# Kernel tuning notes

Measured on AMD Instinct MI355X. Metric: run time of the kernel, lower is better.

Reference implementation:

```python
import jax, jax.numpy as jnp
import numpy as np

BITS = (2, 4, 8)
GROUP = 4
EPS = 1e-5


def _ste_round(x):
    return x + jax.lax.stop_gradient(jnp.round(x) - x)


def _quant_act(x, b):
    s = float(2 ** b - 1)
    return _ste_round(jnp.clip(x, 0.0, 1.0) * s) / s


def _quant_weight(w, mean, std, b):
    # normalize by (mean, std) of the gating-selected channels, then b-bit uniform quant on [-1, 1]
    wn = jnp.clip((w - mean) / (std + EPS), -1.0, 1.0)
    s = float(2 ** b - 1)
    u = _ste_round((wn + 1.0) * 0.5 * s) / s
    return 2.0 * u - 1.0


def _mixed_qconv(x, w, w_mean, w_std, w_logits, a_logits):
    # bitwidth-selectable conv: softmax mixture over quantized weights / activations
    pw = jax.nn.softmax(w_logits)
    pa = jax.nn.softmax(a_logits)
    w_mix = sum(pw[i] * _quant_weight(w, w_mean, w_std, b) for i, b in enumerate(BITS))
    x_mix = sum(pa[i] * _quant_act(x, b) for i, b in enumerate(BITS))
    return jax.lax.conv_general_dilated(
        x_mix, w_mix, window_strides=(1, 1), padding='SAME',
        dimension_numbers=('NCHW', 'OIHW', 'NCHW'))


def _bn(x, g, b, m, v):
    inv = jax.lax.rsqrt(v + EPS)
    return (x - m[None, :, None, None]) * (g * inv)[None, :, None, None] + b[None, :, None, None]


def _masked_mean_std(w, mask):
    # mean/std over gate-selected filter slices; torch uses .data -> stop_gradient, unbiased std
    m = jnp.broadcast_to(mask, w.shape)
    cnt = jnp.sum(m)
    mean = jnp.sum(w * m) / cnt
    var = jnp.sum(m * (w - mean) ** 2) / (cnt - 1.0)
    return jax.lax.stop_gradient(mean), jax.lax.stop_gradient(jnp.sqrt(var))


def _indicator(w1, thr):
    n, c, h, wk = w1.shape
    fw = w1.reshape(n // GROUP, GROUP * c * h * wk)
    nf = fw / jnp.max(jnp.abs(fw))
    norm = jnp.sum(jnp.abs(nf), axis=1) / (GROUP * c * h * wk)  # [n_choices]
    soft = jax.nn.sigmoid(norm - thr)
    hard = (norm > thr).astype(w1.dtype)
    return hard - jax.lax.stop_gradient(soft) + soft  # STE indicator


def setup_inputs() -> dict:
    key = jax.random.key(0)
    ks = jax.random.split(key, 10)
    B, C, H, W = 64, 256, 32, 32
    return {
        'x': jax.random.normal(ks[0], (B, C, H, W), jnp.float32),
        'w1': jax.random.normal(ks[1], (C, C, 3, 3), jnp.float32) * 0.05,
        'w2': jax.random.normal(ks[2], (C, C, 3, 3), jnp.float32) * 0.05,
        'bn1_gamma': jnp.ones((C,), jnp.float32),
        'bn1_beta': jnp.zeros((C,), jnp.float32),
        'bn1_mean': jax.random.normal(ks[3], (C,), jnp.float32) * 0.1,
        'bn1_var': jax.random.uniform(ks[4], (C,), jnp.float32, 0.5, 1.5),
        'bn2_gamma': jnp.ones((C,), jnp.float32),
        'bn2_beta': jnp.zeros((C,), jnp.float32),
        'bn2_mean': jax.random.normal(ks[5], (C,), jnp.float32) * 0.1,
        'bn2_var': jax.random.uniform(ks[6], (C,), jnp.float32, 0.5, 1.5),
        'threshold': jnp.zeros((1,), jnp.float32),
        'w_logits1': jax.random.normal(ks[7], (3,), jnp.float32) * 0.1,
        'a_logits1': jax.random.normal(ks[8], (3,), jnp.float32) * 0.1,
        'w_logits2': jax.random.normal(ks[9], (3,), jnp.float32) * 0.1,
        'a_logits2': jnp.zeros((3,), jnp.float32),
    }


def reference(x, w1, w2, bn1_gamma, bn1_beta, bn1_mean, bn1_var,
              bn2_gamma, bn2_beta, bn2_mean, bn2_var, threshold,
              w_logits1, a_logits1, w_logits2, a_logits2):
    thr = threshold[0]
    ind = _indicator(w1, thr)                       # [n_choices]
    ind_ch = jnp.repeat(ind, GROUP)                 # [out_plane]
    gate_mask = jax.lax.stop_gradient((ind_ch > 0).astype(x.dtype))

    # both_preact path
    residual = x
    h = jax.nn.relu(_bn(x, bn1_gamma, bn1_beta, bn1_mean, bn1_var))
    m1, s1 = _masked_mean_std(w1, gate_mask[:, None, None, None])
    h = _mixed_qconv(h, w1, m1, s1, w_logits1, a_logits1)
    h = jax.nn.relu(_bn(h, bn2_gamma, bn2_beta, bn2_mean, bn2_var))
    m2, s2 = _masked_mean_std(w2, gate_mask[None, :, None, None])
    h = h * ind_ch[None, :, None, None]             # differentiable channel gating
    h = _mixed_qconv(h, w2, m2, s2, w_logits2, a_logits2)
    return h + residual
```

## Files before the change

kernel.cpp:

```cpp
#include <hip/hip_runtime.h>
#include <stdint.h>

#define EPSF 1e-5f

typedef _Float16 h8_t __attribute__((ext_vector_type(8)));
typedef float f4_t __attribute__((ext_vector_type(4)));

#define BB 64
#define CC 256
#define HH 32
#define WW 32
#define HP 34
#define WP 34
#define MTOT (BB*HH*WW)
#define WELEMS (CC*CC*9)
#define PADIMG (HP*WP*CC)
#define PADTOT (BB*PADIMG)

#define S_GSUM   0
#define S_GMAX   64
#define S_W1S    128
#define S_W1Q    192
#define S_W2S    256
#define S_W2Q    320
#define S_M1     384
#define S_SD1    385
#define S_M2     386
#define S_SD2    387
#define S_PW1    388
#define S_PA1    391
#define S_PW2    394
#define S_PA2    397
#define S_INDCH  400
#define S_BN1SC  656
#define S_BN1SH  912
#define S_BN2SC  1168
#define S_BN2SH  1424

#define OFF_STATS 0
#define OFF_A1    8192
#define OFF_A2    (OFF_A1 + PADTOT*2)
#define OFF_W1T   (OFF_A2 + PADTOT*2)
#define OFF_W2T   (OFF_W1T + 9*CC*CC*2)

__device__ __forceinline__ void async_load16(void* lds, const void* g) {
  __builtin_amdgcn_global_load_lds(
      reinterpret_cast<uint32_t __attribute__((address_space(1)))*>((uintptr_t)g),
      reinterpret_cast<uint32_t __attribute__((address_space(3)))*>((uint32_t)(uintptr_t)lds),
      16, 0, 0);
}

__device__ __forceinline__ float wave_sum(float v) {
  for (int o = 32; o; o >>= 1) v += __shfl_down(v, o);
  return v;
}
__device__ __forceinline__ float wave_max(float v) {
  for (int o = 32; o; o >>= 1) v = fmaxf(v, __shfl_down(v, o));
  return v;
}

__device__ __forceinline__ void softmax3(const float* l, float* out) {
  float m = fmaxf(fmaxf(l[0], l[1]), l[2]);
  float e0 = expf(l[0] - m), e1 = expf(l[1] - m), e2 = expf(l[2] - m);
  float inv = 1.f / (e0 + e1 + e2);
  out[0] = e0 * inv; out[1] = e1 * inv; out[2] = e2 * inv;
}

__global__ void k_stats(const float* __restrict__ w1, const float* __restrict__ w2,
                        float* stats) {
  __shared__ float red[4][4];
  int bid = blockIdx.x, t = threadIdx.x;
  int lane = t & 63, w = t >> 6;
  if (bid < 64) {
    const float* p = w1 + bid * 9216;
    float sa = 0.f, s = 0.f, q = 0.f, mx = 0.f;
    for (int i = t; i < 9216; i += 256) {
      float v = p[i];
      float a = fabsf(v);
      sa += a; s += v; q += v * v; mx = fmaxf(mx, a);
    }
    sa = wave_sum(sa); s = wave_sum(s); q = wave_sum(q); mx = wave_max(mx);
    if (lane == 0) { red[w][0] = sa; red[w][1] = s; red[w][2] = q; red[w][3] = mx; }
    __syncthreads();
    if (t == 0) {
      float a = 0, b = 0, c = 0, d = 0;
      for (int k = 0; k < 4; ++k) {
        a += red[k][0]; b += red[k][1]; c += red[k][2]; d = fmaxf(d, red[k][3]);
      }
      stats[S_GSUM + bid] = a;
      stats[S_W1S + bid] = b;
      stats[S_W1Q + bid] = c;
      stats[S_GMAX + bid] = d;
    }
  } else {
    int g = bid - 64;
    const float* p = w2 + (size_t)t * 2304 + g * 36;
    float s = 0.f, q = 0.f;
#pragma unroll
    for (int i = 0; i < 36; ++i) { float v = p[i]; s += v; q += v * v; }
    s = wave_sum(s); q = wave_sum(q);
    if (lane == 0) { red[w][0] = s; red[w][1] = q; }
    __syncthreads();
    if (t == 0) {
      float a = 0, b = 0;
      for (int k = 0; k < 4; ++k) { a += red[k][0]; b += red[k][1]; }
      stats[S_W2S + g] = a;
      stats[S_W2Q + g] = b;
    }
  }
}

__global__ void k_prep2(const float* thr_p,
                        const float* bn1g, const float* bn1b, const float* bn1m, const float* bn1v,
                        const float* bn2g, const float* bn2b, const float* bn2m, const float* bn2v,
                        const float* wl1, const float* al1, const float* wl2, const float* al2,
                        float* stats) {
  int t = threadIdx.x;
  __shared__ float sind[64];
  if (t < 64) {
    float thr = thr_p[0];
    float mx = wave_max(stats[S_GMAX + t]);
    mx = __shfl(mx, 0);
    float norm = stats[S_GSUM + t] / mx / 9216.0f;
    float soft = 1.f / (1.f + expf(-(norm - thr)));
    float hard = (norm > thr) ? 1.f : 0.f;
    float iv = (hard - soft) + soft;
    sind[t] = iv;
    float gate = (iv > 0.f) ? 1.f : 0.f;
    float ng = wave_sum(gate);
    float s1 = wave_sum(gate * stats[S_W1S + t]);
    float q1 = wave_sum(gate * stats[S_W1Q + t]);
    float s2 = wave_sum(gate * stats[S_W2S + t]);
    float q2 = wave_sum(gate * stats[S_W2Q + t]);
    if (t == 0) {
      float cnt = ng * 4.0f * 2304.0f;
      float m1 = s1 / cnt;
      float v1 = (q1 - cnt * m1 * m1) / (cnt - 1.0f);
      stats[S_M1] = m1; stats[S_SD1] = sqrtf(fmaxf(v1, 0.f));
      float m2 = s2 / cnt;
      float v2 = (q2 - cnt * m2 * m2) / (cnt - 1.0f);
      stats[S_M2] = m2; stats[S_SD2] = sqrtf(fmaxf(v2, 0.f));
      softmax3(wl1, stats + S_PW1);
      softmax3(al1, stats + S_PA1);
      softmax3(wl2, stats + S_PW2);
      softmax3(al2, stats + S_PA2);
    }
  }
  __syncthreads();
  stats[S_INDCH + t] = sind[t >> 2];
  float sc1 = bn1g[t] * (1.f / sqrtf(bn1v[t] + EPSF));
  stats[S_BN1SC + t] = sc1;
  stats[S_BN1SH + t] = bn1b[t] - bn1m[t] * sc1;
  float sc2 = bn2g[t] * (1.f / sqrtf(bn2v[t] + EPSF));
  stats[S_BN2SC + t] = sc2;
  stats[S_BN2SH + t] = bn2b[t] - bn2m[t] * sc2;
}

#define WPS 264
__global__ void k_wprep(const float* __restrict__ w1, const float* __restrict__ w2,
                        const float* __restrict__ stats,
                        _Float16* __restrict__ wt1, _Float16* __restrict__ wt2) {
  __shared__ __attribute__((aligned(16))) _Float16 lds[9 * WPS];
  int bid = blockIdx.x;
  int which = bid >> 8, o = bid & 255;
  const float* w = (which ? w2 : w1) + (size_t)o * 2304;
  float mean = stats[which ? S_M2 : S_M1];
  float sd = stats[which ? S_SD2 : S_SD1] + EPSF;
  const float* pw = stats + (which ? S_PW2 : S_PW1);
  float p0 = pw[0], p1 = pw[1], p2 = pw[2];
  int t = threadIdx.x;
#pragma unroll
  for (int it = 0; it < 9; ++it) {
    int f = it * 256 + t;
    float v = w[f];
    float wn = fminf(fmaxf((v - mean) / sd, -1.f), 1.f);
    float u0 = rintf((wn + 1.f) * 0.5f * 3.f) / 3.f;
    float u1 = rintf((wn + 1.f) * 0.5f * 15.f) / 15.f;
    float u2 = rintf((wn + 1.f) * 0.5f * 255.f) / 255.f;
    float mix = p0 * (2.f * u0 - 1.f) + p1 * (2.f * u1 - 1.f) + p2 * (2.f * u2 - 1.f);
    int ci = f / 9;
    int e = f - 9 * ci;
    lds[e * WPS + ci] = (_Float16)mix;
  }
  __syncthreads();
  _Float16* dst0 = (which ? wt2 : wt1) + o * 256;
#pragma unroll
  for (int it = 0; it < 2; ++it) {
    int qid = it * 256 + t;
    if (qid < 288) {
      int e = qid >> 5, c8 = (qid & 31) * 8;
      *(h8_t*)(dst0 + e * 65536 + c8) = *(const h8_t*)(lds + e * WPS + c8);
    }
  }
}

#define APR_STRIDE 264
__global__ void k_aprep(const float* __restrict__ xin, const float* __restrict__ stats,
                        _Float16* __restrict__ a1, _Float16* __restrict__ a2) {
  __shared__ __attribute__((aligned(16))) _Float16 lds[32 * APR_STRIDE];
  int bid = blockIdx.x;
  int t = threadIdx.x;
  if (bid >= BB * HH) {
    int b = bid - BB * HH;
    _Float16* img = (b >= BB ? a2 : a1) + (size_t)(b & 63) * PADIMG;
    uint64_t* u = (uint64_t*)img;
#pragma unroll
    for (int it = 0; it < 17; ++it) {
      int idx = it * 256 + t;
      int r33 = (idx >= 2176);
      u[(size_t)(r33 ? 33 * WP * 64 : 0) + (idx - (r33 ? 2176 : 0))] = 0ull;
    }
#pragma unroll
    for (int it = 0; it < 16; ++it) {
      int idx = it * 256 + t;
      int p = idx >> 6;
      int y = 1 + (p >> 1), x = (p & 1) ? 33 : 0;
      u[(size_t)(y * WP + x) * 64 + (idx & 63)] = 0ull;
    }
    return;
  }
  int n = bid >> 5, y = bid & 31;
  int x4 = (t & 7) * 4, c0 = t >> 3;
  float pa0 = stats[S_PA1], pa1 = stats[S_PA1 + 1], pa2 = stats[S_PA1 + 2];
  const float* bsc = stats + S_BN1SC;
  const float* bsh = stats + S_BN1SH;
#pragma unroll
  for (int it = 0; it < 8; ++it) {
    int c = it * 32 + c0;
    const float* src = xin + ((size_t)(n * CC + c) * HH + y) * WW + x4;
    float4 v = *(const float4*)src;
    float sc = bsc[c], sh = bsh[c];
#pragma unroll
    for (int k = 0; k < 4; ++k) {
      float vv = (&v.x)[k];
      vv = fmaxf(vv * sc + sh, 0.f);
      float cl = fminf(vv, 1.f);
      float q = pa0 * (rintf(cl * 3.f) / 3.f) + pa1 * (rintf(cl * 15.f) / 15.f)
              + pa2 * (rintf(cl * 255.f) / 255.f);
      lds[(x4 + k) * APR_STRIDE + c] = (_Float16)q;
    }
  }
  __syncthreads();
  _Float16* orow = a1 + ((size_t)(n * HP + (y + 1)) * WP + 1) * CC;
#pragma unroll
  for (int it = 0; it < 4; ++it) {
    int qid = it * 256 + t;
    int xx = qid >> 5, c8 = (qid & 31) * 8;
    *(h8_t*)(orow + xx * CC + c8) = *(const h8_t*)(lds + xx * APR_STRIDE + c8);
  }
}

template <bool SW>
__global__ __launch_bounds__(256) void k_conv(
    const _Float16* __restrict__ act,
    const _Float16* __restrict__ wts,
    const float* __restrict__ stats,
    _Float16* __restrict__ a2out,
    const float* __restrict__ resid,
    float* __restrict__ out) {
  __shared__ __attribute__((aligned(16))) _Float16 As[128 * 64];
  __shared__ __attribute__((aligned(16))) _Float16 Ws[128 * 64];
  const int tid = threadIdx.x;
  const int lane = tid & 63, wid = tid >> 6;
  const int xcd = blockIdx.x & 7;
  const int j = blockIdx.x >> 3;
  const int blk_co = j >> 6;
  const int blk_m = xcd * 64 + (j & 63);

  const int srow = wid * 8 + (lane >> 3);
  const int g = (lane & 7) ^ (lane >> 3);
  int abase[4], wbase[4];
#pragma unroll
  for (int q = 0; q < 4; ++q) {
    int r = q * 32 + srow;
    int m = blk_m * 128 + r;
    int n = m >> 10, y = (m >> 5) & 31, x = m & 31;
    abase[q] = ((n * HP + y) * WP + x) * CC + g * 8;
    wbase[q] = (blk_co * 128 + r) * CC + g * 8;
  }

  const int wr = wid >> 1, wc = wid & 1;

  f4_t acc[4][4];
  const f4_t z4 = {0.f, 0.f, 0.f, 0.f};
#pragma unroll
  for (int i = 0; i < 4; ++i)
#pragma unroll
    for (int j2 = 0; j2 < 4; ++j2) acc[i][j2] = z4;

  int raoff[4], rboff[4];
#pragma unroll
  for (int i = 0; i < 4; ++i) {
    int ra = wr * 64 + i * 16 + (lane & 15);
    int sa = (lane >> 4) ^ (lane & 7);
    raoff[i] = ra * 64 + sa * 8;
    int rb = wc * 64 + i * 16 + (lane & 15);
    rboff[i] = rb * 64 + sa * 8;
  }

#pragma unroll 1
  for (int e = 0; e < 9; ++e) {
    const int kh = e / 3, kw = e - 3 * kh;
    const int aoffe = (kh * WP + kw) * CC;
    const int woffe = e * CC * CC;
#pragma unroll
    for (int kc = 0; kc < 4; ++kc) {
      const int ao = aoffe + kc * 64;
      const int wo = woffe + kc * 64;
      __syncthreads();
#pragma unroll
      for (int q = 0; q < 4; ++q) {
        async_load16(As + (q * 32 + wid * 8) * 64, act + abase[q] + ao);
        async_load16(Ws + (q * 32 + wid * 8) * 64, wts + wbase[q] + wo);
      }
      __syncthreads();
      const _Float16* aT = SW ? Ws : As;
      const _Float16* bT = SW ? As : Ws;
#pragma unroll
      for (int kk = 0; kk < 2; ++kk) {
        h8_t fa[4], fb[4];
#pragma unroll
        for (int i = 0; i < 4; ++i) {
          fa[i] = *(const h8_t*)(aT + (raoff[i] ^ (kk * 32)));
          fb[i] = *(const h8_t*)(bT + (rboff[i] ^ (kk * 32)));
        }
#pragma unroll
        for (int i = 0; i < 4; ++i)
#pragma unroll
          for (int j2 = 0; j2 < 4; ++j2)
            acc[i][j2] = __builtin_amdgcn_mfma_f32_16x16x32_f16(fa[i], fb[j2], acc[i][j2], 0, 0, 0);
      }
    }
  }

  const int quad = lane >> 4;
  const int cq = lane & 15;
  if (!SW) {
    const float pa0 = stats[S_PA2], pa1 = stats[S_PA2 + 1], pa2 = stats[S_PA2 + 2];
#pragma unroll
    for (int j2 = 0; j2 < 4; ++j2) {
      const int co = blk_co * 128 + wc * 64 + j2 * 16 + cq;
      const float sc = stats[S_BN2SC + co];
      const float sh = stats[S_BN2SH + co];
      const float ic = stats[S_INDCH + co];
#pragma unroll
      for (int i = 0; i < 4; ++i) {
        const int mbase = blk_m * 128 + wr * 64 + i * 16 + quad * 4;
#pragma unroll
        for (int rg = 0; rg < 4; ++rg) {
          const int m = mbase + rg;
          const int n = m >> 10, y = (m >> 5) & 31, x = m & 31;
          float h = fmaxf(acc[i][j2][rg] * sc + sh, 0.f) * ic;
          float cl = fminf(h, 1.f);
          float q = pa0 * (rintf(cl * 3.f) / 3.f) + pa1 * (rintf(cl * 15.f) / 15.f)
                  + pa2 * (rintf(cl * 255.f) / 255.f);
          a2out[((size_t)(n * HP + y + 1) * WP + (x + 1)) * CC + co] = (_Float16)q;
        }
      }
    }
  } else {
#pragma unroll
    for (int j2 = 0; j2 < 4; ++j2) {
      const int m = blk_m * 128 + wc * 64 + j2 * 16 + cq;
      const int n = m >> 10, y = (m >> 5) & 31, x = m & 31;
#pragma unroll
      for (int i = 0; i < 4; ++i) {
        const int cobase = blk_co * 128 + wr * 64 + i * 16 + quad * 4;
#pragma unroll
        for (int rg = 0; rg < 4; ++rg) {
          const int co = cobase + rg;
          const int idx = ((n * CC + co) << 10) + (y << 5) + x;
          out[idx] = acc[i][j2][rg] + resid[idx];
        }
      }
    }
  }
}

extern "C" void kernel_launch(void* const* d_in, const int* in_sizes, int n_in,
                              void* d_out, int out_size, void* d_ws, size_t ws_size,
                              hipStream_t stream) {
  const float* x    = (const float*)d_in[0];
  const float* w1   = (const float*)d_in[1];
  const float* w2   = (const float*)d_in[2];
  const float* bn1g = (const float*)d_in[3];
  const float* bn1b = (const float*)d_in[4];
  const float* bn1m = (const float*)d_in[5];
  const float* bn1v = (const float*)d_in[6];
  const float* bn2g = (const float*)d_in[7];
  const float* bn2b = (const float*)d_in[8];
  const float* bn2m = (const float*)d_in[9];
  const float* bn2v = (const float*)d_in[10];
  const float* thr  = (const float*)d_in[11];
  const float* wl1  = (const float*)d_in[12];
  const float* al1  = (const float*)d_in[13];
  const float* wl2  = (const float*)d_in[14];
  const float* al2  = (const float*)d_in[15];

  char* ws = (char*)d_ws;
  float* stats = (float*)(ws + OFF_STATS);
  _Float16* a1 = (_Float16*)(ws + OFF_A1);
  _Float16* a2 = (_Float16*)(ws + OFF_A2);
  _Float16* wt1 = (_Float16*)(ws + OFF_W1T);
  _Float16* wt2 = (_Float16*)(ws + OFF_W2T);
  float* out = (float*)d_out;

  k_stats<<<128, 256, 0, stream>>>(w1, w2, stats);
  k_prep2<<<1, 256, 0, stream>>>(thr, bn1g, bn1b, bn1m, bn1v,
                                 bn2g, bn2b, bn2m, bn2v, wl1, al1, wl2, al2, stats);
  k_wprep<<<512, 256, 0, stream>>>(w1, w2, stats, wt1, wt2);
  k_aprep<<<BB * HH + 128, 256, 0, stream>>>(x, stats, a1, a2);
  k_conv<false><<<1024, 256, 0, stream>>>(a1, wt1, stats, a2, nullptr, nullptr);
  k_conv<true><<<1024, 256, 0, stream>>>(a2, wt2, stats, nullptr, x, out);
}
```

Measured before the change: 363.8 us.

## Fuse prep kernels into one launch and reorder conv K-loop channel-major

```diff
diff --git a/kernel.cpp b/kernel.cpp
--- a/kernel.cpp
+++ b/kernel.cpp
@@ -12,8 +12,6 @@
 #define WW 32
 #define HP 34
 #define WP 34
-#define MTOT (BB*HH*WW)
-#define WELEMS (CC*CC*9)
 #define PADIMG (HP*WP*CC)
 #define PADTOT (BB*PADIMG)
 
@@ -23,19 +21,10 @@
 #define S_W1Q    192
 #define S_W2S    256
 #define S_W2Q    320
-#define S_M1     384
-#define S_SD1    385
-#define S_M2     386
-#define S_SD2    387
-#define S_PW1    388
-#define S_PA1    391
-#define S_PW2    394
-#define S_PA2    397
+#define S_PA2    384
 #define S_INDCH  400
-#define S_BN1SC  656
-#define S_BN1SH  912
-#define S_BN2SC  1168
-#define S_BN2SH  1424
+#define S_BN2SC  656
+#define S_BN2SH  912
 
 #define OFF_STATS 0
 #define OFF_A1    8192
@@ -64,6 +53,12 @@
   float e0 = expf(l[0] - m), e1 = expf(l[1] - m), e2 = expf(l[2] - m);
   float inv = 1.f / (e0 + e1 + e2);
   out[0] = e0 * inv; out[1] = e1 * inv; out[2] = e2 * inv;
+}
+
+__device__ __forceinline__ float qmix_act(float v, float p0, float p1, float p2) {
+  float cl = fminf(fmaxf(v, 0.f), 1.f);
+  return p0 * (rintf(cl * 3.f) / 3.f) + p1 * (rintf(cl * 15.f) / 15.f)
+       + p2 * (rintf(cl * 255.f) / 255.f);
 }
 
 __global__ void k_stats(const float* __restrict__ w1, const float* __restrict__ w2,
@@ -110,98 +105,98 @@
   }
 }
 
-__global__ void k_prep2(const float* thr_p,
-                        const float* bn1g, const float* bn1b, const float* bn1m, const float* bn1v,
-                        const float* bn2g, const float* bn2b, const float* bn2m, const float* bn2v,
-                        const float* wl1, const float* al1, const float* wl2, const float* al2,
-                        float* stats) {
-  int t = threadIdx.x;
-  __shared__ float sind[64];
-  if (t < 64) {
-    float thr = thr_p[0];
-    float mx = wave_max(stats[S_GMAX + t]);
-    mx = __shfl(mx, 0);
-    float norm = stats[S_GSUM + t] / mx / 9216.0f;
-    float soft = 1.f / (1.f + expf(-(norm - thr)));
-    float hard = (norm > thr) ? 1.f : 0.f;
-    float iv = (hard - soft) + soft;
-    sind[t] = iv;
-    float gate = (iv > 0.f) ? 1.f : 0.f;
-    float ng = wave_sum(gate);
-    float s1 = wave_sum(gate * stats[S_W1S + t]);
-    float q1 = wave_sum(gate * stats[S_W1Q + t]);
-    float s2 = wave_sum(gate * stats[S_W2S + t]);
-    float q2 = wave_sum(gate * stats[S_W2Q + t]);
-    if (t == 0) {
-      float cnt = ng * 4.0f * 2304.0f;
-      float m1 = s1 / cnt;
-      float v1 = (q1 - cnt * m1 * m1) / (cnt - 1.0f);
-      stats[S_M1] = m1; stats[S_SD1] = sqrtf(fmaxf(v1, 0.f));
-      float m2 = s2 / cnt;
-      float v2 = (q2 - cnt * m2 * m2) / (cnt - 1.0f);
-      stats[S_M2] = m2; stats[S_SD2] = sqrtf(fmaxf(v2, 0.f));
-      softmax3(wl1, stats + S_PW1);
-      softmax3(al1, stats + S_PA1);
-      softmax3(wl2, stats + S_PW2);
-      softmax3(al2, stats + S_PA2);
-    }
-  }
-  __syncthreads();
-  stats[S_INDCH + t] = sind[t >> 2];
-  float sc1 = bn1g[t] * (1.f / sqrtf(bn1v[t] + EPSF));
-  stats[S_BN1SC + t] = sc1;
-  stats[S_BN1SH + t] = bn1b[t] - bn1m[t] * sc1;
-  float sc2 = bn2g[t] * (1.f / sqrtf(bn2v[t] + EPSF));
-  stats[S_BN2SC + t] = sc2;
-  stats[S_BN2SH + t] = bn2b[t] - bn2m[t] * sc2;
-}
-
 #define WPS 264
-__global__ void k_wprep(const float* __restrict__ w1, const float* __restrict__ w2,
-                        const float* __restrict__ stats,
-                        _Float16* __restrict__ wt1, _Float16* __restrict__ wt2) {
-  __shared__ __attribute__((aligned(16))) _Float16 lds[9 * WPS];
-  int bid = blockIdx.x;
-  int which = bid >> 8, o = bid & 255;
-  const float* w = (which ? w2 : w1) + (size_t)o * 2304;
-  float mean = stats[which ? S_M2 : S_M1];
-  float sd = stats[which ? S_SD2 : S_SD1] + EPSF;
-  const float* pw = stats + (which ? S_PW2 : S_PW1);
-  float p0 = pw[0], p1 = pw[1], p2 = pw[2];
-  int t = threadIdx.x;
-#pragma unroll
-  for (int it = 0; it < 9; ++it) {
-    int f = it * 256 + t;
-    float v = w[f];
-    float wn = fminf(fmaxf((v - mean) / sd, -1.f), 1.f);
-    float u0 = rintf((wn + 1.f) * 0.5f * 3.f) / 3.f;
-    float u1 = rintf((wn + 1.f) * 0.5f * 15.f) / 15.f;
-    float u2 = rintf((wn + 1.f) * 0.5f * 255.f) / 255.f;
-    float mix = p0 * (2.f * u0 - 1.f) + p1 * (2.f * u1 - 1.f) + p2 * (2.f * u2 - 1.f);
-    int ci = f / 9;
-    int e = f - 9 * ci;
-    lds[e * WPS + ci] = (_Float16)mix;
-  }
-  __syncthreads();
-  _Float16* dst0 = (which ? wt2 : wt1) + o * 256;
-#pragma unroll
-  for (int it = 0; it < 2; ++it) {
-    int qid = it * 256 + t;
-    if (qid < 288) {
-      int e = qid >> 5, c8 = (qid & 31) * 8;
-      *(h8_t*)(dst0 + e * 65536 + c8) = *(const h8_t*)(lds + e * WPS + c8);
-    }
-  }
-}
-
 #define APR_STRIDE 264
-__global__ void k_aprep(const float* __restrict__ xin, const float* __restrict__ stats,
+__global__ void k_fused(const float* __restrict__ w1, const float* __restrict__ w2,
+                        const float* __restrict__ xin, const float* __restrict__ thr_p,
+                        const float* __restrict__ bn1g, const float* __restrict__ bn1b,
+                        const float* __restrict__ bn1m, const float* __restrict__ bn1v,
+                        const float* __restrict__ bn2g, const float* __restrict__ bn2b,
+                        const float* __restrict__ bn2m, const float* __restrict__ bn2v,
+                        const float* __restrict__ wl1, const float* __restrict__ al1,
+                        const float* __restrict__ wl2, const float* __restrict__ al2,
+                        float* __restrict__ stats,
+                        _Float16* __restrict__ wt1, _Float16* __restrict__ wt2,
                         _Float16* __restrict__ a1, _Float16* __restrict__ a2) {
-  __shared__ __attribute__((aligned(16))) _Float16 lds[32 * APR_STRIDE];
-  int bid = blockIdx.x;
-  int t = threadIdx.x;
-  if (bid >= BB * HH) {
-    int b = bid - BB * HH;
+  int bid = blockIdx.x, t = threadIdx.x;
+
+  if (bid == 0) {
+    __shared__ float sind[64];
+    if (t < 64) {
+      float thr = thr_p[0];
+      float mx = wave_max(stats[S_GMAX + t]);
+      mx = __shfl(mx, 0);
+      float norm = stats[S_GSUM + t] / mx / 9216.0f;
+      float soft = 1.f / (1.f + expf(-(norm - thr)));
+      float hard = (norm > thr) ? 1.f : 0.f;
+      sind[t] = (hard - soft) + soft;
+    }
+    __syncthreads();
+    stats[S_INDCH + t] = sind[t >> 2];
+    float sc2 = bn2g[t] * (1.f / sqrtf(bn2v[t] + EPSF));
+    stats[S_BN2SC + t] = sc2;
+    stats[S_BN2SH + t] = bn2b[t] - bn2m[t] * sc2;
+    if (t == 0) softmax3(al2, stats + S_PA2);
+    return;
+  }
+
+  if (bid <= 512) {
+    __shared__ __attribute__((aligned(16))) _Float16 lds[9 * WPS];
+    __shared__ float sM, sSD, sP[3];
+    int which = (bid - 1) >> 8, o = (bid - 1) & 255;
+    if (t < 64) {
+      float thr = thr_p[0];
+      float mx = wave_max(stats[S_GMAX + t]);
+      mx = __shfl(mx, 0);
+      float norm = stats[S_GSUM + t] / mx / 9216.0f;
+      float soft = 1.f / (1.f + expf(-(norm - thr)));
+      float hard = (norm > thr) ? 1.f : 0.f;
+      float iv = (hard - soft) + soft;
+      float gate = (iv > 0.f) ? 1.f : 0.f;
+      float ng = wave_sum(gate);
+      float s = wave_sum(gate * stats[(which ? S_W2S : S_W1S) + t]);
+      float q = wave_sum(gate * stats[(which ? S_W2Q : S_W1Q) + t]);
+      if (t == 0) {
+        float cnt = ng * 9216.0f;
+        float m = s / cnt;
+        float v = (q - cnt * m * m) / (cnt - 1.0f);
+        sM = m; sSD = sqrtf(fmaxf(v, 0.f));
+        softmax3(which ? wl2 : wl1, sP);
+      }
+    }
+    __syncthreads();
+    const float* w = (which ? w2 : w1) + (size_t)o * 2304;
+    float mean = sM, sd = sSD + EPSF;
+    float p0 = sP[0], p1 = sP[1], p2 = sP[2];
+#pragma unroll
+    for (int it = 0; it < 9; ++it) {
+      int f = it * 256 + t;
+      float v = w[f];
+      float wn = fminf(fmaxf((v - mean) / sd, -1.f), 1.f);
+      float u0 = rintf((wn + 1.f) * 0.5f * 3.f) / 3.f;
+      float u1 = rintf((wn + 1.f) * 0.5f * 15.f) / 15.f;
+      float u2 = rintf((wn + 1.f) * 0.5f * 255.f) / 255.f;
+      float mix = p0 * (2.f * u0 - 1.f) + p1 * (2.f * u1 - 1.f) + p2 * (2.f * u2 - 1.f);
+      int ci = f / 9;
+      int e = f - 9 * ci;
+      lds[e * WPS + ci] = (_Float16)mix;
+    }
+    __syncthreads();
+    _Float16* dst0 = (which ? wt2 : wt1) + o * 256;
+#pragma unroll
+    for (int it = 0; it < 2; ++it) {
+      int qid = it * 256 + t;
+      if (qid < 288) {
+        int e = qid >> 5, c8 = (qid & 31) * 8;
+        *(h8_t*)(dst0 + e * 65536 + c8) = *(const h8_t*)(lds + e * WPS + c8);
+      }
+    }
+    return;
+  }
+
+  int ab = bid - 513;
+  if (ab >= BB * HH) {
+    int b = ab - BB * HH;
     _Float16* img = (b >= BB ? a2 : a1) + (size_t)(b & 63) * PADIMG;
     uint64_t* u = (uint64_t*)img;
 #pragma unroll
@@ -219,24 +214,28 @@
     }
     return;
   }
-  int n = bid >> 5, y = bid & 31;
+
+  __shared__ __attribute__((aligned(16))) _Float16 lds[32 * APR_STRIDE];
+  __shared__ float sBsc[256], sBsh[256], sPa[3];
+  {
+    float sc1 = bn1g[t] * (1.f / sqrtf(bn1v[t] + EPSF));
+    sBsc[t] = sc1;
+    sBsh[t] = bn1b[t] - bn1m[t] * sc1;
+    if (t == 0) softmax3(al1, sPa);
+  }
+  __syncthreads();
+  int n = ab >> 5, y = ab & 31;
   int x4 = (t & 7) * 4, c0 = t >> 3;
-  float pa0 = stats[S_PA1], pa1 = stats[S_PA1 + 1], pa2 = stats[S_PA1 + 2];
-  const float* bsc = stats + S_BN1SC;
-  const float* bsh = stats + S_BN1SH;
+  float pa0 = sPa[0], pa1 = sPa[1], pa2 = sPa[2];
 #pragma unroll
   for (int it = 0; it < 8; ++it) {
     int c = it * 32 + c0;
     const float* src = xin + ((size_t)(n * CC + c) * HH + y) * WW + x4;
     float4 v = *(const float4*)src;
-    float sc = bsc[c], sh = bsh[c];
+    float sc = sBsc[c], sh = sBsh[c];
 #pragma unroll
     for (int k = 0; k < 4; ++k) {
-      float vv = (&v.x)[k];
-      vv = fmaxf(vv * sc + sh, 0.f);
-      float cl = fminf(vv, 1.f);
-      float q = pa0 * (rintf(cl * 3.f) / 3.f) + pa1 * (rintf(cl * 15.f) / 15.f)
-              + pa2 * (rintf(cl * 255.f) / 255.f);
+      float q = qmix_act((&v.x)[k] * sc + sh, pa0, pa1, pa2);
       lds[(x4 + k) * APR_STRIDE + c] = (_Float16)q;
     }
   }
@@ -299,14 +298,13 @@
   }
 
 #pragma unroll 1
-  for (int e = 0; e < 9; ++e) {
-    const int kh = e / 3, kw = e - 3 * kh;
-    const int aoffe = (kh * WP + kw) * CC;
-    const int woffe = e * CC * CC;
-#pragma unroll
-    for (int kc = 0; kc < 4; ++kc) {
-      const int ao = aoffe + kc * 64;
-      const int wo = woffe + kc * 64;
+  for (int kc = 0; kc < 4; ++kc) {
+    const int kb = kc * 64;
+#pragma unroll
+    for (int e = 0; e < 9; ++e) {
+      const int kh = e / 3, kw = e - 3 * kh;
+      const int ao = (kh * WP + kw) * CC + kb;
+      const int wo = e * CC * CC + kb;
       __syncthreads();
 #pragma unroll
       for (int q = 0; q < 4; ++q) {
@@ -351,9 +349,7 @@
           const int m = mbase + rg;
           const int n = m >> 10, y = (m >> 5) & 31, x = m & 31;
           float h = fmaxf(acc[i][j2][rg] * sc + sh, 0.f) * ic;
-          float cl = fminf(h, 1.f);
-          float q = pa0 * (rintf(cl * 3.f) / 3.f) + pa1 * (rintf(cl * 15.f) / 15.f)
-                  + pa2 * (rintf(cl * 255.f) / 255.f);
+          float q = qmix_act(h, pa0, pa1, pa2);
           a2out[((size_t)(n * HP + y + 1) * WP + (x + 1)) * CC + co] = (_Float16)q;
         }
       }
@@ -406,10 +402,9 @@
   float* out = (float*)d_out;
 
   k_stats<<<128, 256, 0, stream>>>(w1, w2, stats);
-  k_prep2<<<1, 256, 0, stream>>>(thr, bn1g, bn1b, bn1m, bn1v,
-                                 bn2g, bn2b, bn2m, bn2v, wl1, al1, wl2, al2, stats);
-  k_wprep<<<512, 256, 0, stream>>>(w1, w2, stats, wt1, wt2);
-  k_aprep<<<BB * HH + 128, 256, 0, stream>>>(x, stats, a1, a2);
+  k_fused<<<1 + 512 + BB * HH + 128, 256, 0, stream>>>(
+      w1, w2, x, thr, bn1g, bn1b, bn1m, bn1v, bn2g, bn2b, bn2m, bn2v,
+      wl1, al1, wl2, al2, stats, wt1, wt2, a1, a2);
   k_conv<false><<<1024, 256, 0, stream>>>(a1, wt1, stats, a2, nullptr, nullptr);
   k_conv<true><<<1024, 256, 0, stream>>>(a2, wt2, stats, nullptr, x, out);
 }
```

Measured after the change: 340.9 us. -6.3%, faster.
